# Performance work log

Measured on AMD Instinct MI355X. Metric: run time of the kernel, lower is better.

## Reference

```python
import jax, jax.numpy as jnp
import numpy as np

N_POINTS = 4096
N_PROJS = 2000


def setup_inputs() -> dict:
    key = jax.random.key(0)
    k1, k2, k3 = jax.random.split(key, 3)
    Xs = jax.random.normal(k1, (N_POINTS, 3), dtype=jnp.float32)
    Xt = jax.random.normal(k2, (N_POINTS, 3), dtype=jnp.float32)
    Us = jax.random.normal(k3, (N_PROJS, 3, 2), dtype=jnp.float32)
    return {"Xs": Xs, "Xt": Xt, "Us": Us}


def _project_to_circle(X, Us):
    # X: [n, d], Us: [P, d, 2] -> angles in [0, 1): [P, n]
    Xp = jnp.einsum('pdk,nd->pnk', Us, X)  # [P, n, 2]
    nrm = jnp.sqrt(jnp.sum(Xp * Xp, axis=-1, keepdims=True))
    Xp = Xp / jnp.maximum(nrm, 1e-12)  # F.normalize
    return (jnp.arctan2(-Xp[..., 1], -Xp[..., 0]) + np.pi) / (2 * np.pi)


def _emd1d_circle_p1(u_values, v_values):
    # Circular W1 via level-median (Delon et al.). u,v: [P, n], [P, m]
    P, n = u_values.shape
    m = v_values.shape[-1]
    dt = u_values.dtype
    u_w = jnp.full((P, n), 1.0 / n, dtype=dt)
    v_w = jnp.full((P, m), 1.0 / m, dtype=dt)
    us = jnp.sort(u_values, axis=-1)
    vs = jnp.sort(v_values, axis=-1)
    vals = jnp.concatenate([us, vs], axis=-1)            # [P, n+m]
    sorter = jnp.argsort(vals, axis=-1)
    vals_sorted = jnp.take_along_axis(vals, sorter, axis=-1)
    w_cat = jnp.concatenate([u_w, -v_w], axis=-1)
    cdf_diff = jnp.cumsum(jnp.take_along_axis(w_cat, sorter, axis=-1), axis=-1)
    cdf_sorter = jnp.argsort(cdf_diff, axis=-1)
    cdf_diff_sorted = jnp.take_along_axis(cdf_diff, cdf_sorter, axis=-1)
    vals_pad = jnp.concatenate([vals_sorted, jnp.ones((P, 1), dtype=dt)], axis=-1)
    delta = vals_pad[..., 1:] - vals_pad[..., :-1]
    weight_sorted = jnp.take_along_axis(delta, cdf_sorter, axis=-1)
    sum_weights = jnp.cumsum(weight_sorted, axis=-1) - 0.5
    sum_weights = jnp.where(sum_weights < 0, jnp.inf, sum_weights)
    inds = jnp.argmin(sum_weights, axis=-1)
    levMed = jnp.take_along_axis(cdf_diff_sorted, inds[:, None], axis=-1)  # [P, 1]
    return jnp.sum(delta * jnp.abs(cdf_diff - levMed), axis=-1)  # [P]


def reference(Xs, Xt, Us):
    Xps = _project_to_circle(Xs, Us)  # [P, n]
    Xpt = _project_to_circle(Xt, Us)  # [P, m]
    w1 = _emd1d_circle_p1(Xps, Xpt)
    return jnp.mean(w1)
```

## Files before the change

kernel.cpp:

```cpp
#include <hip/hip_runtime.h>
#include <math.h>

#define NPTS   4096
#define NPROJ  2000
#define NB     256
#define NMERGE 8192
#define VPT    32

__device__ __forceinline__ int sw(int i) {
    return (i & ~31) | ((i + (i >> 5)) & 31);
}

__device__ __forceinline__ void local_merge(float v[VPT], bool asc) {
    #pragma unroll
    for (int j = 16; j >= 1; j >>= 1) {
        #pragma unroll
        for (int e = 0; e < VPT; ++e) {
            if ((e & j) == 0) {
                float a = v[e], b = v[e | j];
                float mn = fminf(a, b), mx = fmaxf(a, b);
                v[e]     = asc ? mn : mx;
                v[e | j] = asc ? mx : mn;
            }
        }
    }
}

__global__ __launch_bounds__(NB, 2) void swd_kernel(
    const float* __restrict__ Xs, const float* __restrict__ Xt,
    const float* __restrict__ Us, float* __restrict__ out)
{
    __shared__ float keys[NMERGE];

    const int tid  = threadIdx.x;
    const int arr  = tid >> 7;
    const int c    = tid & 127;
    const int lane = tid & 63;
    const int wid  = tid >> 6;
    const int p    = blockIdx.x;

    const float u00 = Us[p*6+0], u01 = Us[p*6+1];
    const float u10 = Us[p*6+2], u11 = Us[p*6+3];
    const float u20 = Us[p*6+4], u21 = Us[p*6+5];

    const float pi_f   = 3.14159265358979323846f;
    const float inv2pi = 0.15915494309189535f;

    const float* __restrict__ X = arr ? Xt : Xs;

    float v[VPT];
    {
        const float4* X4 = (const float4*)(X + c * (VPT * 3));
        #pragma unroll
        for (int t = 0; t < 8; ++t) {
            float4 q0 = X4[t*3+0], q1 = X4[t*3+1], q2 = X4[t*3+2];
            #define ANG(x,y,z) ((atan2f(-((x)*u01+(y)*u11+(z)*u21), \
                                        -((x)*u00+(y)*u10+(z)*u20)) + pi_f) * inv2pi)
            v[t*4+0] = ANG(q0.x, q0.y, q0.z);
            v[t*4+1] = ANG(q0.w, q1.x, q1.y);
            v[t*4+2] = ANG(q1.z, q1.w, q2.x);
            v[t*4+3] = ANG(q2.y, q2.z, q2.w);
            #undef ANG
        }
    }

    #pragma unroll
    for (int k = 2; k <= 16; k <<= 1) {
        #pragma unroll
        for (int j = k >> 1; j >= 1; j >>= 1) {
            #pragma unroll
            for (int e = 0; e < VPT; ++e) {
                if ((e & j) == 0) {
                    bool asc = ((e & k) == 0);
                    float a = v[e], b = v[e | j];
                    float mn = fminf(a, b), mx = fmaxf(a, b);
                    v[e]     = asc ? mn : mx;
                    v[e | j] = asc ? mx : mn;
                }
            }
        }
    }

    local_merge(v, (c & 1) == 0);

    #pragma unroll
    for (int k = 64; k <= 2048; k <<= 1) {
        bool asc = ((c & (k >> 5)) == 0);
        #pragma unroll
        for (int d = k >> 6; d >= 1; d >>= 1) {
            bool keepmin = (((c & d) == 0) == asc);
            #pragma unroll
            for (int e = 0; e < VPT; ++e) {
                float o = __shfl_xor(v[e], d, 64);
                v[e] = keepmin ? fminf(v[e], o) : fmaxf(v[e], o);
            }
        }
        local_merge(v, asc);
    }

    #pragma unroll
    for (int e = 0; e < VPT; ++e) keys[sw(tid * VPT + e)] = v[e];
    __syncthreads();
    {
        const int pbase = (tid ^ 64) * VPT;
        const bool keepmin = (c & 64) == 0;
        #pragma unroll
        for (int e = 0; e < VPT; ++e) {
            float o = keys[sw(pbase + e)];
            v[e] = keepmin ? fminf(v[e], o) : fmaxf(v[e], o);
        }
    }
    __syncthreads();
    #pragma unroll
    for (int d = 32; d >= 1; d >>= 1) {
        bool keepmin = ((c & d) == 0);
        #pragma unroll
        for (int e = 0; e < VPT; ++e) {
            float o = __shfl_xor(v[e], d, 64);
            v[e] = keepmin ? fminf(v[e], o) : fmaxf(v[e], o);
        }
    }
    local_merge(v, true);

    #pragma unroll
    for (int e = 0; e < VPT; ++e) keys[sw(tid * VPT + e)] = v[e];
    __syncthreads();

    int c_init;
    int offmin = 64, offmax = -64;
    unsigned int c8[8] = {0,0,0,0,0,0,0,0};
    {
        const int d0 = tid * VPT;
        int lo = d0 > NPTS ? d0 - NPTS : 0;
        int hi = d0 < NPTS ? d0 : NPTS;
        while (lo < hi) {
            int mid = (lo + hi) >> 1;
            if (keys[sw(mid)] <= keys[sw(NPTS + (d0 - 1 - mid))]) lo = mid + 1; else hi = mid;
        }
        int i = lo, j = d0 - lo;
        c_init = i - j;
        const float FMAXV = 3.402823466e+38f;
        float cu = (i < NPTS) ? keys[sw(i)] : FMAXV;
        float cv = (j < NPTS) ? keys[sw(NPTS + j)] : FMAXV;
        #pragma unroll
        for (int s = 0; s < VPT; ++s) {
            float cur;
            if (cu <= cv) { cur = cu; ++i; cu = (i < NPTS) ? keys[sw(i)] : FMAXV; }
            else          { cur = cv; ++j; cv = (j < NPTS) ? keys[sw(NPTS + j)] : FMAXV; }
            float nxt = fminf(cu, cv);
            if (nxt == FMAXV) nxt = 1.0f;
            v[s] = nxt - cur;
            int off = (i - j) - c_init;
            offmin = min(offmin, off);
            offmax = max(offmax, off);
            c8[s >> 2] |= ((unsigned int)(off & 0xff)) << ((s & 3) * 8);
        }
    }

    __syncthreads();
    int*   ired = (int*)keys;
    float* red  = keys + 8;

    int cmn = c_init + offmin, cmx = c_init + offmax;
    #pragma unroll
    for (int o = 32; o >= 1; o >>= 1) {
        cmn = min(cmn, __shfl_xor(cmn, o, 64));
        cmx = max(cmx, __shfl_xor(cmx, o, 64));
    }
    if (lane == 0) { ired[wid] = cmn; ired[4 + wid] = cmx; }
    __syncthreads();
    cmn = min(min(ired[0], ired[1]), min(ired[2], ired[3]));
    cmx = max(max(ired[4], ired[5]), max(ired[6], ired[7]));

    int lo_c = cmn - 1, hi_c = cmx;
    int it = 0;
    #pragma unroll 1
    while (hi_c - lo_c > 1) {
        const int mid = (lo_c + hi_c) >> 1;
        const int thr = mid - c_init;
        float s_loc = 0.0f;
        #pragma unroll
        for (int s = 0; s < VPT; ++s) {
            int off = (int)(c8[s >> 2] << ((3 - (s & 3)) * 8)) >> 24;
            s_loc += (off <= thr) ? v[s] : 0.0f;
        }
        #pragma unroll
        for (int o = 32; o >= 1; o >>= 1) s_loc += __shfl_down(s_loc, o, 64);
        if (lane == 0) red[it * 4 + wid] = s_loc;
        __syncthreads();
        float S = red[it*4+0] + red[it*4+1] + red[it*4+2] + red[it*4+3];
        if (S >= 0.5f) hi_c = mid; else lo_c = mid;
        ++it;
    }
    const int cstar = hi_c;

    float part = 0.0f;
    {
        const int thr = cstar - c_init;
        #pragma unroll
        for (int s = 0; s < VPT; ++s) {
            int off = (int)(c8[s >> 2] << ((3 - (s & 3)) * 8)) >> 24;
            part += v[s] * fabsf((float)(off - thr));
        }
    }
    #pragma unroll
    for (int o = 32; o >= 1; o >>= 1) part += __shfl_down(part, o, 64);
    if (lane == 0) red[56 + wid] = part;
    __syncthreads();
    if (tid == 0) {
        float w1 = (red[56] + red[57] + red[58] + red[59]) * (1.0f / 4096.0f);
        atomicAdd(out, w1 * (1.0f / (float)NPROJ));
    }
}

extern "C" void kernel_launch(void* const* d_in, const int* in_sizes, int n_in,
                              void* d_out, int out_size, void* d_ws, size_t ws_size,
                              hipStream_t stream) {
    const float* Xs = (const float*)d_in[0];
    const float* Xt = (const float*)d_in[1];
    const float* Us = (const float*)d_in[2];
    float* out = (float*)d_out;

    hipMemsetAsync(out, 0, sizeof(float), stream);
    swd_kernel<<<NPROJ, NB, 0, stream>>>(Xs, Xt, Us, out);
}
```

Measured before the change: 243.1 us.

## Double threads per block and halve per-thread elements in bitonic sort

Raises the block to 512 threads with 16 values per thread instead of 256 threads with 32. The bitonic network is restructured to match: extra LDS exchange stages cover cross-wavefront distances of 64 and 128, and the reductions now span 8 wavefronts. The aim is to cut register pressure and the serial per-thread work in the merge scan, giving more parallelism per projection. In exchange it adds more __syncthreads and LDS round trips, plus more merge-path binary searches.

```diff
diff --git a/kernel.cpp b/kernel.cpp
--- a/kernel.cpp
+++ b/kernel.cpp
@@ -3,9 +3,9 @@
 
 #define NPTS   4096
 #define NPROJ  2000
-#define NB     256
+#define NB     512
 #define NMERGE 8192
-#define VPT    32
+#define VPT    16
 
 __device__ __forceinline__ int sw(int i) {
     return (i & ~31) | ((i + (i >> 5)) & 31);
@@ -13,7 +13,7 @@
 
 __device__ __forceinline__ void local_merge(float v[VPT], bool asc) {
     #pragma unroll
-    for (int j = 16; j >= 1; j >>= 1) {
+    for (int j = 8; j >= 1; j >>= 1) {
         #pragma unroll
         for (int e = 0; e < VPT; ++e) {
             if ((e & j) == 0) {
@@ -26,15 +26,15 @@
     }
 }
 
-__global__ __launch_bounds__(NB, 2) void swd_kernel(
+__global__ __launch_bounds__(NB) void swd_kernel(
     const float* __restrict__ Xs, const float* __restrict__ Xt,
     const float* __restrict__ Us, float* __restrict__ out)
 {
     __shared__ float keys[NMERGE];
 
     const int tid  = threadIdx.x;
-    const int arr  = tid >> 7;
-    const int c    = tid & 127;
+    const int arr  = tid >> 8;
+    const int c    = tid & 255;
     const int lane = tid & 63;
     const int wid  = tid >> 6;
     const int p    = blockIdx.x;
@@ -52,7 +52,7 @@
     {
         const float4* X4 = (const float4*)(X + c * (VPT * 3));
         #pragma unroll
-        for (int t = 0; t < 8; ++t) {
+        for (int t = 0; t < 4; ++t) {
             float4 q0 = X4[t*3+0], q1 = X4[t*3+1], q2 = X4[t*3+2];
             #define ANG(x,y,z) ((atan2f(-((x)*u01+(y)*u11+(z)*u21), \
                                         -((x)*u00+(y)*u10+(z)*u20)) + pi_f) * inv2pi)
@@ -65,7 +65,7 @@
     }
 
     #pragma unroll
-    for (int k = 2; k <= 16; k <<= 1) {
+    for (int k = 2; k <= 8; k <<= 1) {
         #pragma unroll
         for (int j = k >> 1; j >= 1; j >>= 1) {
             #pragma unroll
@@ -84,10 +84,10 @@
     local_merge(v, (c & 1) == 0);
 
     #pragma unroll
-    for (int k = 64; k <= 2048; k <<= 1) {
-        bool asc = ((c & (k >> 5)) == 0);
-        #pragma unroll
-        for (int d = k >> 6; d >= 1; d >>= 1) {
+    for (int k = 32; k <= 1024; k <<= 1) {
+        bool asc = ((c & (k >> 4)) == 0);
+        #pragma unroll
+        for (int d = k >> 5; d >= 1; d >>= 1) {
             bool keepmin = (((c & d) == 0) == asc);
             #pragma unroll
             for (int e = 0; e < VPT; ++e) {
@@ -98,19 +98,38 @@
         local_merge(v, asc);
     }
 
-    #pragma unroll
-    for (int e = 0; e < VPT; ++e) keys[sw(tid * VPT + e)] = v[e];
-    __syncthreads();
-    {
-        const int pbase = (tid ^ 64) * VPT;
-        const bool keepmin = (c & 64) == 0;
-        #pragma unroll
-        for (int e = 0; e < VPT; ++e) {
-            float o = keys[sw(pbase + e)];
-            v[e] = keepmin ? fminf(v[e], o) : fmaxf(v[e], o);
-        }
-    }
-    __syncthreads();
+    #define LDS_XCHG(PXOR, KEEPMIN_EXPR)                                   \
+    {                                                                      \
+        _Pragma("unroll")                                                  \
+        for (int e = 0; e < VPT; ++e) keys[sw(tid * VPT + e)] = v[e];      \
+        __syncthreads();                                                   \
+        const int pbase = (tid ^ (PXOR)) * VPT;                            \
+        const bool keepmin = (KEEPMIN_EXPR);                               \
+        _Pragma("unroll")                                                  \
+        for (int e = 0; e < VPT; ++e) {                                    \
+            float o = keys[sw(pbase + e)];                                 \
+            v[e] = keepmin ? fminf(v[e], o) : fmaxf(v[e], o);              \
+        }                                                                  \
+        __syncthreads();                                                   \
+    }
+
+    {
+        bool asc = ((c & 128) == 0);
+        LDS_XCHG(64, ((c & 64) == 0) == asc);
+        #pragma unroll
+        for (int d = 32; d >= 1; d >>= 1) {
+            bool keepmin = (((c & d) == 0) == asc);
+            #pragma unroll
+            for (int e = 0; e < VPT; ++e) {
+                float o = __shfl_xor(v[e], d, 64);
+                v[e] = keepmin ? fminf(v[e], o) : fmaxf(v[e], o);
+            }
+        }
+        local_merge(v, asc);
+    }
+
+    LDS_XCHG(128, (c & 128) == 0);
+    LDS_XCHG(64,  (c & 64) == 0);
     #pragma unroll
     for (int d = 32; d >= 1; d >>= 1) {
         bool keepmin = ((c & d) == 0);
@@ -121,14 +140,15 @@
         }
     }
     local_merge(v, true);
+    #undef LDS_XCHG
 
     #pragma unroll
     for (int e = 0; e < VPT; ++e) keys[sw(tid * VPT + e)] = v[e];
     __syncthreads();
 
     int c_init;
-    int offmin = 64, offmax = -64;
-    unsigned int c8[8] = {0,0,0,0,0,0,0,0};
+    int offmin = 32, offmax = -32;
+    unsigned int c8[4] = {0,0,0,0};
     {
         const int d0 = tid * VPT;
         int lo = d0 > NPTS ? d0 - NPTS : 0;
@@ -159,7 +179,7 @@
 
     __syncthreads();
     int*   ired = (int*)keys;
-    float* red  = keys + 8;
+    float* red  = keys + 16;
 
     int cmn = c_init + offmin, cmx = c_init + offmax;
     #pragma unroll
@@ -167,10 +187,16 @@
         cmn = min(cmn, __shfl_xor(cmn, o, 64));
         cmx = max(cmx, __shfl_xor(cmx, o, 64));
     }
-    if (lane == 0) { ired[wid] = cmn; ired[4 + wid] = cmx; }
-    __syncthreads();
-    cmn = min(min(ired[0], ired[1]), min(ired[2], ired[3]));
-    cmx = max(max(ired[4], ired[5]), max(ired[6], ired[7]));
+    if (lane == 0) { ired[wid] = cmn; ired[8 + wid] = cmx; }
+    __syncthreads();
+    {
+        int a0 = min(min(ired[0], ired[1]), min(ired[2], ired[3]));
+        int a1 = min(min(ired[4], ired[5]), min(ired[6], ired[7]));
+        cmn = min(a0, a1);
+        int b0 = max(max(ired[8], ired[9]),  max(ired[10], ired[11]));
+        int b1 = max(max(ired[12], ired[13]), max(ired[14], ired[15]));
+        cmx = max(b0, b1);
+    }
 
     int lo_c = cmn - 1, hi_c = cmx;
     int it = 0;
@@ -186,9 +212,11 @@
         }
         #pragma unroll
         for (int o = 32; o >= 1; o >>= 1) s_loc += __shfl_down(s_loc, o, 64);
-        if (lane == 0) red[it * 4 + wid] = s_loc;
+        if (lane == 0) red[it * 8 + wid] = s_loc;
         __syncthreads();
-        float S = red[it*4+0] + red[it*4+1] + red[it*4+2] + red[it*4+3];
+        float S = 0.0f;
+        #pragma unroll
+        for (int w = 0; w < 8; ++w) S += red[it * 8 + w];
         if (S >= 0.5f) hi_c = mid; else lo_c = mid;
         ++it;
     }
@@ -205,10 +233,13 @@
     }
     #pragma unroll
     for (int o = 32; o >= 1; o >>= 1) part += __shfl_down(part, o, 64);
-    if (lane == 0) red[56 + wid] = part;
+    if (lane == 0) red[15 * 8 + wid] = part;
     __syncthreads();
     if (tid == 0) {
-        float w1 = (red[56] + red[57] + red[58] + red[59]) * (1.0f / 4096.0f);
+        float w1 = 0.0f;
+        #pragma unroll
+        for (int w = 0; w < 8; ++w) w1 += red[15 * 8 + w];
+        w1 *= (1.0f / 4096.0f);
         atomicAdd(out, w1 * (1.0f / (float)NPROJ));
     }
 }
```

After: 230.1 us. -5.3%, faster.
